# Optimization experiments

Measured on AMD Instinct MI355X. Metric: run time of the kernel, lower is better.

## Reference

```python
import jax, jax.numpy as jnp
import numpy as np

B, G, T = 4096, 100, 24


def _greedy_dispatch(demand, caps, prices, slack_price):
    """Exact LP solution of: min prices@alloc + slack_price*slack
    s.t. 0<=alloc<=caps, sum(alloc)+slack = demand (per b,t).
    demand: [B,T] (nonneg), caps: [B,G,T], prices: [G], slack_price: scalar.
    Returns alloc [B,G,T], slack [B,T].
    """
    prices_all = jnp.concatenate([prices, slack_price[None]])        # [G+1]
    # slack capacity = demand itself (slack alone can absorb everything)
    caps_all = jnp.concatenate([caps, demand[:, None, :]], axis=1)    # [B,G+1,T]
    order = jnp.argsort(prices_all)                                   # merit order
    caps_s = caps_all[:, order, :]
    before = jnp.cumsum(caps_s, axis=1) - caps_s                      # capacity ahead in merit order
    alloc_s = jnp.clip(demand[:, None, :] - before, 0.0, caps_s)
    inv = jnp.argsort(order)
    alloc = alloc_s[:, inv, :]
    return alloc[:, :-1, :], alloc[:, -1, :]


def setup_inputs() -> dict:
    key = jax.random.key(0)
    k1, k2, k3, k4 = jax.random.split(key, 4)
    R_up = jax.random.uniform(k1, (B, G, T), dtype=jnp.float32)
    R_dn = jax.random.uniform(k2, (B, G, T), dtype=jnp.float32)
    omega_true = jax.random.normal(k3, (B, T), dtype=jnp.float32) * 5.0
    b_G = 10.0 + 40.0 * jax.random.uniform(k4, (G,), dtype=jnp.float32)  # marginal costs $/MWh
    return {
        "R_up": R_up,
        "R_dn": R_dn,
        "omega_true": omega_true,
        "b_G": b_G,
        "voll": jnp.float32(1000.0),
        "vosp": jnp.float32(500.0),
        "rt_up_ratio": jnp.float32(1.5),
        "rt_dn_ratio": jnp.float32(1.2),
    }


def reference(R_up, R_dn, omega_true, b_G, voll, vosp, rt_up_ratio, rt_dn_ratio):
    c_up = rt_up_ratio * b_G                                          # [G]
    c_dn = rt_dn_ratio * b_G                                          # [G]
    dem_up = jnp.maximum(omega_true, 0.0)                             # [B,T]
    dem_dn = jnp.maximum(-omega_true, 0.0)
    du, LS = _greedy_dispatch(dem_up, R_up, c_up, voll)
    dd, SP = _greedy_dispatch(dem_dn, R_dn, c_dn, vosp)
    rt_obj = (jnp.einsum('g,bgt->b', c_up, du)
              + jnp.einsum('g,bgt->b', c_dn, dd)
              + voll * LS.sum(axis=1) + vosp * SP.sum(axis=1))        # [B]
    return du, dd, LS, SP, rt_obj
```

## Files before the change

kernel.cpp:

```cpp
#include <hip/hip_runtime.h>

#define G_ 100
#define T_ 24
#define GP1 101
#define NB 4
#define BLOCK 256
#define TILE (G_ * T_)
#define VPB (TILE / 4)
#define TSTRIDE 2416
#define PASS_F (NB * TSTRIDE)
#define NVEC 19
#define NACT (2 * NB * T_)

typedef float vfloat4 __attribute__((ext_vector_type(4)));

template<int N>
__device__ __forceinline__ void scan_chunk(int k0,
    float* __restrict__ tile, const int* __restrict__ ordp,
    const float* __restrict__ prp, float dem,
    float& before, float& objp, float& slackv)
{
    int gg[N]; float pr[N], cap[N];
#pragma unroll
    for (int j = 0; j < N; ++j) { gg[j] = ordp[k0 + j]; pr[j] = prp[k0 + j]; }
#pragma unroll
    for (int j = 0; j < N; ++j) {
        int gl = (gg[j] < G_) ? gg[j] : 0;
        cap[j] = tile[gl * T_];
    }
#pragma unroll
    for (int j = 0; j < N; ++j) {
        float c = (gg[j] == G_) ? dem : cap[j];
        float a = fminf(fmaxf(dem - before, 0.f), c);
        before += c;
        objp = fmaf(pr[j], a, objp);
        if (gg[j] == G_) slackv = a;
        else             tile[gg[j] * T_] = a;
    }
}

__global__ __launch_bounds__(BLOCK, 2) void dispatch_kernel(
    const float* __restrict__ R_up, const float* __restrict__ R_dn,
    const float* __restrict__ omega, const float* __restrict__ b_G,
    const float* __restrict__ voll, const float* __restrict__ vosp,
    const float* __restrict__ ru, const float* __restrict__ rd,
    float* __restrict__ out, int B)
{
    __shared__ float s_tile[2 * PASS_F];
    __shared__ float s_praw[2][GP1];
    __shared__ int   s_ord[2][GP1];
    __shared__ float s_pr[2][GP1];
    __shared__ float s_obj[NACT];

    const int tid = threadIdx.x;
    const int b0  = blockIdx.x * NB;
    const size_t bgt = (size_t)B * TILE;

    if (tid < GP1) {
        if (tid < G_) {
            float bg = b_G[tid];
            s_praw[0][tid] = ru[0] * bg;
            s_praw[1][tid] = rd[0] * bg;
        } else {
            s_praw[0][tid] = voll[0];
            s_praw[1][tid] = vosp[0];
        }
    }
    __syncthreads();

    vfloat4 buf[NVEC];
#pragma unroll
    for (int j = 0; j < NVEC; ++j) {
        int i = tid + j * BLOCK;
        if (i < 2 * NB * VPB) {
            int pass = i / (NB * VPB);
            int rem  = i - pass * (NB * VPB);
            int bb   = rem / VPB;
            int v    = rem - bb * VPB;
            const vfloat4* src = pass ? (const vfloat4*)R_dn : (const vfloat4*)R_up;
            buf[j] = src[(size_t)(b0 + bb) * VPB + v];
        }
    }

    const int p    = tid / (NB * T_);
    const int rm   = tid - p * (NB * T_);
    const int bb_s = rm / T_;
    const int t    = rm - bb_s * T_;
    float om = 0.f;
    if (tid < NACT) om = omega[(size_t)(b0 + bb_s) * T_ + t];

    if (tid < GP1) {
        float mu = s_praw[0][tid], md = s_praw[1][tid];
        int r0 = 0, r1 = 0;
        for (int j = 0; j < GP1; ++j) {
            float vu = s_praw[0][j], vd = s_praw[1][j];
            r0 += (vu < mu) || (vu == mu && j < tid);
            r1 += (vd < md) || (vd == md && j < tid);
        }
        s_ord[0][r0] = tid; s_pr[0][r0] = mu;
        s_ord[1][r1] = tid; s_pr[1][r1] = md;
    }

#pragma unroll
    for (int j = 0; j < NVEC; ++j) {
        int i = tid + j * BLOCK;
        if (i < 2 * NB * VPB) {
            int pass = i / (NB * VPB);
            int rem  = i - pass * (NB * VPB);
            int bb   = rem / VPB;
            int v    = rem - bb * VPB;
            *(vfloat4*)&s_tile[pass * PASS_F + bb * TSTRIDE + v * 4] = buf[j];
        }
    }
    __syncthreads();

    if (tid < NACT) {
        const float dem = p ? fmaxf(-om, 0.f) : fmaxf(om, 0.f);
        float* __restrict__ tile = &s_tile[p * PASS_F + bb_s * TSTRIDE + t];
        const int*   __restrict__ ordp = s_ord[p];
        const float* __restrict__ prp  = s_pr[p];
        float before = 0.f, objp = 0.f, slackv = 0.f;
        scan_chunk<16>( 0, tile, ordp, prp, dem, before, objp, slackv);
        scan_chunk<16>(16, tile, ordp, prp, dem, before, objp, slackv);
        scan_chunk<16>(32, tile, ordp, prp, dem, before, objp, slackv);
        scan_chunk<16>(48, tile, ordp, prp, dem, before, objp, slackv);
        scan_chunk<16>(64, tile, ordp, prp, dem, before, objp, slackv);
        scan_chunk<16>(80, tile, ordp, prp, dem, before, objp, slackv);
        scan_chunk< 5>(96, tile, ordp, prp, dem, before, objp, slackv);

        out[2 * bgt + (size_t)p * B * T_ + (size_t)(b0 + bb_s) * T_ + t] = slackv;
        s_obj[tid] = objp;
    }
    __syncthreads();

    if (tid < NB) {
        float s = 0.f;
        for (int j = 0; j < T_; ++j)
            s += s_obj[tid * T_ + j] + s_obj[NB * T_ + tid * T_ + j];
        out[2 * bgt + 2 * (size_t)B * T_ + b0 + tid] = s;
    }

#pragma unroll
    for (int j = 0; j < NVEC; ++j) {
        int i = tid + j * BLOCK;
        if (i < 2 * NB * VPB) {
            int pass = i / (NB * VPB);
            int rem  = i - pass * (NB * VPB);
            int bb   = rem / VPB;
            int v    = rem - bb * VPB;
            vfloat4 val = *(const vfloat4*)&s_tile[pass * PASS_F + bb * TSTRIDE + v * 4];
            vfloat4* dst = (vfloat4*)(out + (size_t)pass * bgt + (size_t)(b0 + bb) * TILE) + v;
            __builtin_nontemporal_store(val, dst);
        }
    }
}

extern "C" void kernel_launch(void* const* d_in, const int* in_sizes, int n_in,
                              void* d_out, int out_size, void* d_ws, size_t ws_size,
                              hipStream_t stream)
{
    const float* R_up  = (const float*)d_in[0];
    const float* R_dn  = (const float*)d_in[1];
    const float* omega = (const float*)d_in[2];
    const float* b_G   = (const float*)d_in[3];
    const float* voll  = (const float*)d_in[4];
    const float* vosp  = (const float*)d_in[5];
    const float* ru    = (const float*)d_in[6];
    const float* rd    = (const float*)d_in[7];

    const int B = in_sizes[0] / TILE;
    float* out = (float*)d_out;

    dispatch_kernel<<<B / NB, BLOCK, 0, stream>>>(
        R_up, R_dn, omega, b_G, voll, vosp, ru, rd, out, B);
}
```

Baseline: 189.2 us.

## Process one batch element per block with smaller LDS tile and higher occupancy

```diff
diff --git a/kernel.cpp b/kernel.cpp
--- a/kernel.cpp
+++ b/kernel.cpp
@@ -3,14 +3,11 @@
 #define G_ 100
 #define T_ 24
 #define GP1 101
-#define NB 4
-#define BLOCK 256
 #define TILE (G_ * T_)
 #define VPB (TILE / 4)
-#define TSTRIDE 2416
-#define PASS_F (NB * TSTRIDE)
-#define NVEC 19
-#define NACT (2 * NB * T_)
+#define BLOCK 256
+#define NACT (2 * T_)
+#define NIT 3
 
 typedef float vfloat4 __attribute__((ext_vector_type(4)));
 
@@ -39,21 +36,21 @@
     }
 }
 
-__global__ __launch_bounds__(BLOCK, 2) void dispatch_kernel(
+__global__ __launch_bounds__(BLOCK, 7) void dispatch_kernel(
     const float* __restrict__ R_up, const float* __restrict__ R_dn,
     const float* __restrict__ omega, const float* __restrict__ b_G,
     const float* __restrict__ voll, const float* __restrict__ vosp,
     const float* __restrict__ ru, const float* __restrict__ rd,
     float* __restrict__ out, int B)
 {
-    __shared__ float s_tile[2 * PASS_F];
+    __shared__ float s_tile[2 * TILE];
     __shared__ float s_praw[2][GP1];
     __shared__ int   s_ord[2][GP1];
     __shared__ float s_pr[2][GP1];
     __shared__ float s_obj[NACT];
 
     const int tid = threadIdx.x;
-    const int b0  = blockIdx.x * NB;
+    const int b   = blockIdx.x;
     const size_t bgt = (size_t)B * TILE;
 
     if (tid < GP1) {
@@ -68,26 +65,18 @@
     }
     __syncthreads();
 
-    vfloat4 buf[NVEC];
+    vfloat4 buf[2][NIT];
+    {
+        const vfloat4* s0 = (const vfloat4*)R_up + (size_t)b * VPB;
+        const vfloat4* s1 = (const vfloat4*)R_dn + (size_t)b * VPB;
 #pragma unroll
-    for (int j = 0; j < NVEC; ++j) {
-        int i = tid + j * BLOCK;
-        if (i < 2 * NB * VPB) {
-            int pass = i / (NB * VPB);
-            int rem  = i - pass * (NB * VPB);
-            int bb   = rem / VPB;
-            int v    = rem - bb * VPB;
-            const vfloat4* src = pass ? (const vfloat4*)R_dn : (const vfloat4*)R_up;
-            buf[j] = src[(size_t)(b0 + bb) * VPB + v];
+        for (int it = 0; it < NIT; ++it) {
+            int i = tid + it * BLOCK;
+            if (i < VPB) { buf[0][it] = s0[i]; buf[1][it] = s1[i]; }
         }
     }
-
-    const int p    = tid / (NB * T_);
-    const int rm   = tid - p * (NB * T_);
-    const int bb_s = rm / T_;
-    const int t    = rm - bb_s * T_;
     float om = 0.f;
-    if (tid < NACT) om = omega[(size_t)(b0 + bb_s) * T_ + t];
+    if (tid < NACT) om = omega[(size_t)b * T_ + (tid % T_)];
 
     if (tid < GP1) {
         float mu = s_praw[0][tid], md = s_praw[1][tid];
@@ -102,21 +91,20 @@
     }
 
 #pragma unroll
-    for (int j = 0; j < NVEC; ++j) {
-        int i = tid + j * BLOCK;
-        if (i < 2 * NB * VPB) {
-            int pass = i / (NB * VPB);
-            int rem  = i - pass * (NB * VPB);
-            int bb   = rem / VPB;
-            int v    = rem - bb * VPB;
-            *(vfloat4*)&s_tile[pass * PASS_F + bb * TSTRIDE + v * 4] = buf[j];
+    for (int it = 0; it < NIT; ++it) {
+        int i = tid + it * BLOCK;
+        if (i < VPB) {
+            *(vfloat4*)&s_tile[i * 4]        = buf[0][it];
+            *(vfloat4*)&s_tile[TILE + i * 4] = buf[1][it];
         }
     }
     __syncthreads();
 
     if (tid < NACT) {
+        const int p = tid / T_;
+        const int t = tid - p * T_;
         const float dem = p ? fmaxf(-om, 0.f) : fmaxf(om, 0.f);
-        float* __restrict__ tile = &s_tile[p * PASS_F + bb_s * TSTRIDE + t];
+        float* __restrict__ tile = &s_tile[p * TILE + t];
         const int*   __restrict__ ordp = s_ord[p];
         const float* __restrict__ prp  = s_pr[p];
         float before = 0.f, objp = 0.f, slackv = 0.f;
@@ -128,29 +116,27 @@
         scan_chunk<16>(80, tile, ordp, prp, dem, before, objp, slackv);
         scan_chunk< 5>(96, tile, ordp, prp, dem, before, objp, slackv);
 
-        out[2 * bgt + (size_t)p * B * T_ + (size_t)(b0 + bb_s) * T_ + t] = slackv;
+        out[2 * bgt + (size_t)p * B * T_ + (size_t)b * T_ + t] = slackv;
         s_obj[tid] = objp;
     }
     __syncthreads();
 
-    if (tid < NB) {
+    if (tid == 0) {
         float s = 0.f;
-        for (int j = 0; j < T_; ++j)
-            s += s_obj[tid * T_ + j] + s_obj[NB * T_ + tid * T_ + j];
-        out[2 * bgt + 2 * (size_t)B * T_ + b0 + tid] = s;
+        for (int j = 0; j < NACT; ++j) s += s_obj[j];
+        out[2 * bgt + 2 * (size_t)B * T_ + b] = s;
     }
 
+    {
+        vfloat4* d0 = (vfloat4*)out + (size_t)b * VPB;
+        vfloat4* d1 = (vfloat4*)(out + bgt) + (size_t)b * VPB;
 #pragma unroll
-    for (int j = 0; j < NVEC; ++j) {
-        int i = tid + j * BLOCK;
-        if (i < 2 * NB * VPB) {
-            int pass = i / (NB * VPB);
-            int rem  = i - pass * (NB * VPB);
-            int bb   = rem / VPB;
-            int v    = rem - bb * VPB;
-            vfloat4 val = *(const vfloat4*)&s_tile[pass * PASS_F + bb * TSTRIDE + v * 4];
-            vfloat4* dst = (vfloat4*)(out + (size_t)pass * bgt + (size_t)(b0 + bb) * TILE) + v;
-            __builtin_nontemporal_store(val, dst);
+        for (int it = 0; it < NIT; ++it) {
+            int i = tid + it * BLOCK;
+            if (i < VPB) {
+                d0[i] = *(const vfloat4*)&s_tile[i * 4];
+                d1[i] = *(const vfloat4*)&s_tile[TILE + i * 4];
+            }
         }
     }
 }
@@ -171,6 +157,6 @@
     const int B = in_sizes[0] / TILE;
     float* out = (float*)d_out;
 
-    dispatch_kernel<<<B / NB, BLOCK, 0, stream>>>(
+    dispatch_kernel<<<B, BLOCK, 0, stream>>>(
         R_up, R_dn, omega, b_G, voll, vosp, ru, rd, out, B);
 }
```

Result: slower. 387.1 us (+104.6%).
